# Performance work log

Measured on AMD Instinct MI355X. Metric: run time of the kernel, lower is better.

## Reference

```python
import jax, jax.numpy as jnp
import numpy as np

NUM_EMB = 512
LATENT = 20


def setup_inputs() -> dict:
    key = jax.random.key(0)
    ks = jax.random.split(key, 10)
    B = 262144
    c = jax.random.normal(ks[0], (B, 100), dtype=jnp.float32)
    W1 = jax.random.normal(ks[1], (100, 200), dtype=jnp.float32) * 0.1
    b1 = jnp.zeros((200,), dtype=jnp.float32)
    W2 = jax.random.normal(ks[2], (200, LATENT), dtype=jnp.float32) * 0.07
    b2 = jnp.zeros((LATENT,), dtype=jnp.float32)
    # codebook initialized uniform(-1/K, 1/K) as in torch
    codebook = jax.random.uniform(ks[3], (NUM_EMB, LATENT), dtype=jnp.float32,
                                  minval=-1.0 / NUM_EMB, maxval=1.0 / NUM_EMB)
    Wmu = jax.random.normal(ks[4], (LATENT, LATENT), dtype=jnp.float32) * 0.2
    bmu = jnp.zeros((LATENT,), dtype=jnp.float32)
    Wlv = jax.random.normal(ks[5], (LATENT, LATENT), dtype=jnp.float32) * 0.2
    blv = jnp.zeros((LATENT,), dtype=jnp.float32)
    return {"c": c, "W1": W1, "b1": b1, "W2": W2, "b2": b2,
            "codebook": codebook, "Wmu": Wmu, "bmu": bmu, "Wlv": Wlv, "blv": blv}


def reference(c, W1, b1, W2, b2, codebook, Wmu, bmu, Wlv, blv):
    # encoder: Linear -> ELU -> Linear
    h = jax.nn.elu(c @ W1 + b1)            # [B, 200]
    z_e = h @ W2 + b2                      # [B, 20]

    # vector quantization: pairwise squared distances to codebook
    d = (jnp.sum(z_e ** 2, axis=1, keepdims=True)
         + jnp.sum(codebook ** 2, axis=1)
         - 2.0 * z_e @ codebook.T)         # [B, K]
    idx = jnp.argmin(d, axis=1)            # [B]
    quantized = codebook[idx]              # [B, 20] gather

    commitment_loss = 0.25 * jnp.mean((jax.lax.stop_gradient(quantized) - z_e) ** 2)
    quantization_loss = jnp.mean((quantized - jax.lax.stop_gradient(z_e)) ** 2)
    z_q = z_e + jax.lax.stop_gradient(quantized - z_e)  # straight-through

    mu_c = z_e @ Wmu + bmu
    logvar_c = z_e @ Wlv + blv
    return (mu_c, logvar_c, z_q, z_e, quantization_loss, commitment_loss)
```

## Files before the change

kernel.cpp:

```cpp
#include <hip/hip_runtime.h>

typedef __bf16 bf16x8 __attribute__((ext_vector_type(8)));
typedef __bf16 bf16x4 __attribute__((ext_vector_type(4)));
typedef float  f32x4  __attribute__((ext_vector_type(4)));
typedef float  f32x2  __attribute__((ext_vector_type(2)));

constexpr int BN  = 262144;
constexpr int DIN = 100;
constexpr int DH  = 200;
constexpr int DZ  = 20;
constexpr int KCB = 512;

constexpr size_t WS_W1F  = 0;
constexpr size_t WS_W2F  = 53248;
constexpr size_t WS_CBF  = 69632;
constexpr size_t WS_WMUF = 102400;
constexpr size_t WS_WLVF = 104448;
constexpr size_t WS_B1P  = 106496;
constexpr size_t WS_B2P  = 107520;
constexpr size_t WS_BMUP = 107648;
constexpr size_t WS_BLVP = 107776;
constexpr size_t WS_PART = 107904;

constexpr int PN_W1 = 26624, PN_W2 = 8192, PN_CB = 16384, PN_WMU = 1024, PN_WLV = 1024;
constexpr int PN_TOT = PN_W1 + PN_W2 + PN_CB + PN_WMU + PN_WLV + 256 + 32 + 32 + 32;

__device__ __forceinline__ unsigned umin2(unsigned a, unsigned b) { return a < b ? a : b; }

__global__ __launch_bounds__(256) void prep_kernel(
    const float* __restrict__ W1, const float* __restrict__ b1,
    const float* __restrict__ W2, const float* __restrict__ b2,
    const float* __restrict__ cb,
    const float* __restrict__ Wmu, const float* __restrict__ bmu,
    const float* __restrict__ Wlv, const float* __restrict__ blv,
    unsigned char* __restrict__ ws)
{
    int e = blockIdx.x * 256 + threadIdx.x;
    if (e >= PN_TOT) return;
    __bf16* w1f  = (__bf16*)(ws + WS_W1F);
    __bf16* w2f  = (__bf16*)(ws + WS_W2F);
    __bf16* cbf  = (__bf16*)(ws + WS_CBF);
    __bf16* wmuf = (__bf16*)(ws + WS_WMUF);
    __bf16* wlvf = (__bf16*)(ws + WS_WLVF);
    float* b1p  = (float*)(ws + WS_B1P);
    float* b2p  = (float*)(ws + WS_B2P);
    float* bmup = (float*)(ws + WS_BMUP);
    float* blvp = (float*)(ws + WS_BLVP);

    if (e < PN_W1) {
        int j = e & 7, lane = (e >> 3) & 63, kk = (e >> 9) & 3, m = e >> 11;
        int n = m * 16 + (lane & 15);
        int k = kk * 32 + ((lane >> 4) << 3) + j;
        w1f[e] = (__bf16)((n < DH && k < DIN) ? W1[k * DH + n] : 0.f);
        return;
    }
    e -= PN_W1;
    if (e < PN_W2) {
        int j = e & 7, lane = (e >> 3) & 63, kk = (e >> 9) & 7, m2 = e >> 12;
        int n = m2 * 16 + (lane & 15);
        int k = kk * 32 + ((lane >> 4) << 3) + j;
        w2f[e] = (__bf16)((n < DZ && k < DH) ? W2[k * DZ + n] : 0.f);
        return;
    }
    e -= PN_W2;
    if (e < PN_CB) {
        int j = e & 7, lane = (e >> 3) & 63, ct = e >> 9;
        int code = ct * 16 + (lane & 15);
        int d = ((lane >> 4) << 3) + j;
        float v = 0.f;
        if (d < DZ) v = -2.f * cb[code * DZ + d];
        else if (d == DZ) {
            float s = 0.f;
            #pragma unroll
            for (int dd = 0; dd < DZ; ++dd) s = fmaf(cb[code * DZ + dd], cb[code * DZ + dd], s);
            v = s;
        }
        cbf[e] = (__bf16)v;
        return;
    }
    e -= PN_CB;
    if (e < PN_WMU) {
        int j = e & 7, lane = (e >> 3) & 63, m2 = e >> 9;
        int n = m2 * 16 + (lane & 15);
        int k = ((lane >> 4) << 3) + j;
        wmuf[e] = (__bf16)((n < DZ && k < DZ) ? Wmu[k * DZ + n] : 0.f);
        return;
    }
    e -= PN_WMU;
    if (e < PN_WLV) {
        int j = e & 7, lane = (e >> 3) & 63, m2 = e >> 9;
        int n = m2 * 16 + (lane & 15);
        int k = ((lane >> 4) << 3) + j;
        wlvf[e] = (__bf16)((n < DZ && k < DZ) ? Wlv[k * DZ + n] : 0.f);
        return;
    }
    e -= PN_WLV;
    if (e < 256) { b1p[e] = (e < DH) ? b1[e] : 0.f; return; }
    e -= 256;
    if (e < 32) { b2p[e] = (e < DZ) ? b2[e] : 0.f; return; }
    e -= 32;
    if (e < 32) { bmup[e] = (e < DZ) ? bmu[e] : 0.f; return; }
    e -= 32;
    blvp[e - 32] = (e - 32 < DZ) ? blv[e - 32] : 0.f;
}

__global__ __launch_bounds__(128) void fused_main(
    const float* __restrict__ c, const float* __restrict__ cb,
    const unsigned char* __restrict__ ws, float* __restrict__ out,
    float* __restrict__ partials)
{
    __shared__ __align__(16) unsigned char region[16384];

    const __bf16* w1f  = (const __bf16*)(ws + WS_W1F);
    const __bf16* w2f  = (const __bf16*)(ws + WS_W2F);
    const __bf16* cbf  = (const __bf16*)(ws + WS_CBF);
    const __bf16* wmuf = (const __bf16*)(ws + WS_WMUF);
    const __bf16* wlvf = (const __bf16*)(ws + WS_WLVF);
    const float* b1p  = (const float*)(ws + WS_B1P);
    const float* b2p  = (const float*)(ws + WS_B2P);
    const float* bmup = (const float*)(ws + WS_BMUP);
    const float* blvp = (const float*)(ws + WS_BLVP);

    const int tid = threadIdx.x;
    const int l   = tid & 63;
    const int wid = __builtin_amdgcn_readfirstlane(tid >> 6);
    const int g   = l >> 4;
    const int li  = l & 15;
    const int rowB = blockIdx.x * 64;

    {
        const float4* cbase = (const float4*)(c + (size_t)rowB * DIN);
        #pragma unroll
        for (int i = 0; i < 13; ++i) {
            int f4 = tid + i * 128;
            if (i < 12 || tid < 64) {
                float4 v = cbase[f4];
                int row = f4 / 25;
                int k4  = (f4 - row * 25) * 4;
                bf16x4 p;
                p[0] = (__bf16)v.x; p[1] = (__bf16)v.y;
                p[2] = (__bf16)v.z; p[3] = (__bf16)v.w;
                int byte = (k4 * 2) ^ ((row & 7) << 4);
                *(bf16x4*)(region + row * 256 + byte) = p;
            }
        }
        #pragma unroll
        for (int i = 0; i < 4; ++i) {
            int e = tid + i * 128;
            if (e < 448) {
                int row = e / 7, s = e - row * 7;
                int byte = (200 + s * 8) ^ ((row & 7) << 4);
                *(uint2*)(region + row * 256 + byte) = uint2{0u, 0u};
            }
        }
    }
    __syncthreads();

    bf16x8 cf0[4], cf1[4];
    #pragma unroll
    for (int nt = 0; nt < 2; ++nt) {
        const int row = wid * 32 + nt * 16 + li;
        const unsigned char* rb = region + row * 256;
        const int swz = (row & 7) << 4;
        #pragma unroll
        for (int kk = 0; kk < 4; ++kk) {
            bf16x8 a = *(const bf16x8*)(rb + ((kk * 64 + g * 16) ^ swz));
            if (nt == 0) cf0[kk] = a; else cf1[kk] = a;
        }
    }

    f32x4 zm0n0, zm0n1, zm1n0, zm1n1;
    {
        f32x4 bz0 = *(const f32x4*)(b2p + g * 4);
        f32x4 bz1 = *(const f32x4*)(b2p + 16 + g * 4);
        zm0n0 = bz0; zm0n1 = bz0; zm1n0 = bz1; zm1n1 = bz1;
    }

    unsigned char* hW = region + wid * 8192;
    const int swzH = (li & 7) << 4;

    #pragma unroll
    for (int hf = 0; hf < 2; ++hf) {
        #pragma unroll
        for (int t = 0; t < 8; ++t) {
            const int mg = hf * 8 + t;
            const int cbyte = (t * 32 + g * 8) ^ swzH;
            if (mg <= 12) {
                f32x4 acc0 = *(const f32x4*)(b1p + mg * 16 + g * 4);
                f32x4 acc1 = acc0;
                #pragma unroll
                for (int kk = 0; kk < 4; ++kk) {
                    bf16x8 aw = *(const bf16x8*)(w1f + ((mg * 4 + kk) * 512 + l * 8));
                    acc0 = __builtin_amdgcn_mfma_f32_16x16x32_bf16(aw, cf0[kk], acc0, 0, 0, 0);
                    acc1 = __builtin_amdgcn_mfma_f32_16x16x32_bf16(aw, cf1[kk], acc1, 0, 0, 0);
                }
                bf16x4 p0, p1;
                #pragma unroll
                for (int r = 0; r < 4; ++r) {
                    float h0 = acc0[r]; h0 = h0 > 0.f ? h0 : (__expf(h0) - 1.f);
                    float h1 = acc1[r]; h1 = h1 > 0.f ? h1 : (__expf(h1) - 1.f);
                    p0[r] = (__bf16)h0; p1[r] = (__bf16)h1;
                }
                *(bf16x4*)(hW + li * 256 + cbyte)        = p0;
                *(bf16x4*)(hW + (li + 16) * 256 + cbyte) = p1;
            } else {
                *(uint2*)(hW + li * 256 + cbyte)        = uint2{0u, 0u};
                *(uint2*)(hW + (li + 16) * 256 + cbyte) = uint2{0u, 0u};
            }
        }
        #pragma unroll
        for (int kk = 0; kk < 4; ++kk) {
            const int kk2 = hf * 4 + kk;
            const int rb = (kk * 64 + g * 16) ^ swzH;
            bf16x8 hb0 = *(const bf16x8*)(hW + li * 256 + rb);
            bf16x8 hb1 = *(const bf16x8*)(hW + (li + 16) * 256 + rb);
            bf16x8 w20 = *(const bf16x8*)(w2f + ((0 * 8 + kk2) * 512 + l * 8));
            bf16x8 w21 = *(const bf16x8*)(w2f + ((1 * 8 + kk2) * 512 + l * 8));
            zm0n0 = __builtin_amdgcn_mfma_f32_16x16x32_bf16(w20, hb0, zm0n0, 0, 0, 0);
            zm0n1 = __builtin_amdgcn_mfma_f32_16x16x32_bf16(w20, hb1, zm0n1, 0, 0, 0);
            zm1n0 = __builtin_amdgcn_mfma_f32_16x16x32_bf16(w21, hb0, zm1n0, 0, 0, 0);
            zm1n1 = __builtin_amdgcn_mfma_f32_16x16x32_bf16(w21, hb1, zm1n1, 0, 0, 0);
        }
    }

    unsigned char* zB = hW;
    const int swzZ = (li & 3) << 4;
    {
        bf16x4 q;
        #pragma unroll
        for (int r = 0; r < 4; ++r) q[r] = (__bf16)zm0n0[r];
        *(bf16x4*)(zB + li * 64 + ((g * 8) ^ swzZ)) = q;
        #pragma unroll
        for (int r = 0; r < 4; ++r) q[r] = (__bf16)zm0n1[r];
        *(bf16x4*)(zB + (li + 16) * 64 + ((g * 8) ^ swzZ)) = q;
        bf16x4 t0;
        #pragma unroll
        for (int r = 0; r < 4; ++r) t0[r] = (__bf16)0.f;
        bf16x4 t1 = t0;
        if (g == 0) {
            #pragma unroll
            for (int r = 0; r < 4; ++r) { t0[r] = (__bf16)zm1n0[r]; t1[r] = (__bf16)zm1n1[r]; }
        } else if (g == 1) { t0[0] = (__bf16)1.0f; t1[0] = (__bf16)1.0f; }
        *(bf16x4*)(zB + li * 64 + ((32 + g * 8) ^ swzZ)) = t0;
        *(bf16x4*)(zB + (li + 16) * 64 + ((32 + g * 8) ^ swzZ)) = t1;
    }

    bf16x8 za0 = *(const bf16x8*)(zB + li * 64 + ((g * 16) ^ swzZ));
    bf16x8 za1 = *(const bf16x8*)(zB + (li + 16) * 64 + ((g * 16) ^ swzZ));
    __syncthreads();

    unsigned run0 = 0xFFFFFFFFu, run1 = 0xFFFFFFFFu;
    f32x4 one4;
    one4[0] = 1.f; one4[1] = 1.f; one4[2] = 1.f; one4[3] = 1.f;
    #pragma unroll 8
    for (int ct = 0; ct < 32; ++ct) {
        bf16x8 cf = *(const bf16x8*)(cbf + (ct * 512 + l * 8));
        f32x4 s0 = __builtin_amdgcn_mfma_f32_16x16x32_bf16(cf, za0, one4, 0, 0, 0);
        f32x4 s1 = __builtin_amdgcn_mfma_f32_16x16x32_bf16(cf, za1, one4, 0, 0, 0);
        const unsigned ib = (unsigned)(ct * 16 + g * 4);
        unsigned k0 = (__float_as_uint(s0[0]) & ~511u) | (ib + 0);
        unsigned k1 = (__float_as_uint(s0[1]) & ~511u) | (ib + 1);
        unsigned k2 = (__float_as_uint(s0[2]) & ~511u) | (ib + 2);
        unsigned k3 = (__float_as_uint(s0[3]) & ~511u) | (ib + 3);
        run0 = umin2(umin2(k0, k1), umin2(umin2(k2, k3), run0));
        k0 = (__float_as_uint(s1[0]) & ~511u) | (ib + 0);
        k1 = (__float_as_uint(s1[1]) & ~511u) | (ib + 1);
        k2 = (__float_as_uint(s1[2]) & ~511u) | (ib + 2);
        k3 = (__float_as_uint(s1[3]) & ~511u) | (ib + 3);
        run1 = umin2(umin2(k0, k1), umin2(umin2(k2, k3), run1));
    }
    run0 = umin2(run0, (unsigned)__shfl_xor((int)run0, 16, 64));
    run0 = umin2(run0, (unsigned)__shfl_xor((int)run0, 32, 64));
    run1 = umin2(run1, (unsigned)__shfl_xor((int)run1, 16, 64));
    run1 = umin2(run1, (unsigned)__shfl_xor((int)run1, 32, 64));
    const int idx0 = (int)(run0 & 511u);
    const int idx1 = (int)(run1 & 511u);

    const size_t SEC = (size_t)BN * DZ;
    const size_t obase = (size_t)rowB * DZ;
    float* o_mu = out + obase;
    float* o_lv = out + SEC + obase;
    float* o_zq = out + 2 * SEC + obase;
    float* o_ze = out + 3 * SEC + obase;

    float* sA = (float*)region;
    float* sB = (float*)region + 1280;
    const int r0 = wid * 32 + li, r1 = r0 + 16;

    {
        f32x4 bm0 = *(const f32x4*)(bmup + g * 4);
        f32x4 bm1 = *(const f32x4*)(bmup + 16 + g * 4);
        bf16x8 wm0 = *(const bf16x8*)(wmuf + (0 * 512 + l * 8));
        bf16x8 wm1 = *(const bf16x8*)(wmuf + (1 * 512 + l * 8));
        f32x4 a00 = __builtin_amdgcn_mfma_f32_16x16x32_bf16(wm0, za0, bm0, 0, 0, 0);
        f32x4 a01 = __builtin_amdgcn_mfma_f32_16x16x32_bf16(wm0, za1, bm0, 0, 0, 0);
        f32x4 a10 = __builtin_amdgcn_mfma_f32_16x16x32_bf16(wm1, za0, bm1, 0, 0, 0);
        f32x4 a11 = __builtin_amdgcn_mfma_f32_16x16x32_bf16(wm1, za1, bm1, 0, 0, 0);
        *(float4*)(sA + r0 * DZ + g * 4) = *(float4*)&a00;
        *(float4*)(sA + r1 * DZ + g * 4) = *(float4*)&a01;
        if (g == 0) {
            *(float4*)(sA + r0 * DZ + 16) = *(float4*)&a10;
            *(float4*)(sA + r1 * DZ + 16) = *(float4*)&a11;
        }
    }
    {
        f32x4 bv0 = *(const f32x4*)(blvp + g * 4);
        f32x4 bv1 = *(const f32x4*)(blvp + 16 + g * 4);
        bf16x8 wl0 = *(const bf16x8*)(wlvf + (0 * 512 + l * 8));
        bf16x8 wl1 = *(const bf16x8*)(wlvf + (1 * 512 + l * 8));
        f32x4 a00 = __builtin_amdgcn_mfma_f32_16x16x32_bf16(wl0, za0, bv0, 0, 0, 0);
        f32x4 a01 = __builtin_amdgcn_mfma_f32_16x16x32_bf16(wl0, za1, bv0, 0, 0, 0);
        f32x4 a10 = __builtin_amdgcn_mfma_f32_16x16x32_bf16(wl1, za0, bv1, 0, 0, 0);
        f32x4 a11 = __builtin_amdgcn_mfma_f32_16x16x32_bf16(wl1, za1, bv1, 0, 0, 0);
        *(float4*)(sB + r0 * DZ + g * 4) = *(float4*)&a00;
        *(float4*)(sB + r1 * DZ + g * 4) = *(float4*)&a01;
        if (g == 0) {
            *(float4*)(sB + r0 * DZ + 16) = *(float4*)&a10;
            *(float4*)(sB + r1 * DZ + 16) = *(float4*)&a11;
        }
    }
    __syncthreads();
    #pragma unroll
    for (int i = 0; i < 5; ++i) {
        int w = tid * 2 + i * 256;
        __builtin_nontemporal_store(*(const f32x2*)(sA + w), (f32x2*)(o_mu + w));
        __builtin_nontemporal_store(*(const f32x2*)(sB + w), (f32x2*)(o_lv + w));
    }
    __syncthreads();

    float lsum = 0.f;
    {
        float4 q00 = *(const float4*)(cb + idx0 * DZ + g * 4);
        float4 q10 = *(const float4*)(cb + idx1 * DZ + g * 4);
        *(float4*)(sA + r0 * DZ + g * 4) = q00;
        *(float4*)(sA + r1 * DZ + g * 4) = q10;
        *(float4*)(sB + r0 * DZ + g * 4) = *(float4*)&zm0n0;
        *(float4*)(sB + r1 * DZ + g * 4) = *(float4*)&zm0n1;
        float d;
        d = q00.x - zm0n0[0]; lsum = fmaf(d, d, lsum);
        d = q00.y - zm0n0[1]; lsum = fmaf(d, d, lsum);
        d = q00.z - zm0n0[2]; lsum = fmaf(d, d, lsum);
        d = q00.w - zm0n0[3]; lsum = fmaf(d, d, lsum);
        d = q10.x - zm0n1[0]; lsum = fmaf(d, d, lsum);
        d = q10.y - zm0n1[1]; lsum = fmaf(d, d, lsum);
        d = q10.z - zm0n1[2]; lsum = fmaf(d, d, lsum);
        d = q10.w - zm0n1[3]; lsum = fmaf(d, d, lsum);
        if (g == 0) {
            float4 qe0 = *(const float4*)(cb + idx0 * DZ + 16);
            float4 qe1 = *(const float4*)(cb + idx1 * DZ + 16);
            *(float4*)(sA + r0 * DZ + 16) = qe0;
            *(float4*)(sA + r1 * DZ + 16) = qe1;
            *(float4*)(sB + r0 * DZ + 16) = *(float4*)&zm1n0;
            *(float4*)(sB + r1 * DZ + 16) = *(float4*)&zm1n1;
            d = qe0.x - zm1n0[0]; lsum = fmaf(d, d, lsum);
            d = qe0.y - zm1n0[1]; lsum = fmaf(d, d, lsum);
            d = qe0.z - zm1n0[2]; lsum = fmaf(d, d, lsum);
            d = qe0.w - zm1n0[3]; lsum = fmaf(d, d, lsum);
            d = qe1.x - zm1n1[0]; lsum = fmaf(d, d, lsum);
            d = qe1.y - zm1n1[1]; lsum = fmaf(d, d, lsum);
            d = qe1.z - zm1n1[2]; lsum = fmaf(d, d, lsum);
            d = qe1.w - zm1n1[3]; lsum = fmaf(d, d, lsum);
        }
    }
    #pragma unroll
    for (int off = 32; off > 0; off >>= 1) lsum += __shfl_down(lsum, off, 64);
    if (l == 0) partials[blockIdx.x * 2 + wid] = lsum;
    __syncthreads();
    #pragma unroll
    for (int i = 0; i < 5; ++i) {
        int w = tid * 2 + i * 256;
        __builtin_nontemporal_store(*(const f32x2*)(sA + w), (f32x2*)(o_zq + w));
        __builtin_nontemporal_store(*(const f32x2*)(sB + w), (f32x2*)(o_ze + w));
    }
}

__global__ __launch_bounds__(256) void loss_reduce(const float* __restrict__ partials,
                                                   float* __restrict__ out_scalars) {
    int t = threadIdx.x;
    float s = 0.f;
    #pragma unroll
    for (int i = 0; i < 32; ++i) s += partials[t + 256 * i];
    #pragma unroll
    for (int off = 32; off > 0; off >>= 1) s += __shfl_down(s, off, 64);
    __shared__ float wsum[4];
    if ((t & 63) == 0) wsum[t >> 6] = s;
    __syncthreads();
    if (t == 0) {
        float total = (wsum[0] + wsum[1]) + (wsum[2] + wsum[3]);
        float ql = total / (float)((size_t)BN * DZ);
        out_scalars[0] = ql;
        out_scalars[1] = 0.25f * ql;
    }
}

extern "C" void kernel_launch(void* const* d_in, const int* in_sizes, int n_in,
                              void* d_out, int out_size, void* d_ws, size_t ws_size,
                              hipStream_t stream) {
    const float* c   = (const float*)d_in[0];
    const float* W1  = (const float*)d_in[1];
    const float* b1  = (const float*)d_in[2];
    const float* W2  = (const float*)d_in[3];
    const float* b2  = (const float*)d_in[4];
    const float* cb  = (const float*)d_in[5];
    const float* Wmu = (const float*)d_in[6];
    const float* bmu = (const float*)d_in[7];
    const float* Wlv = (const float*)d_in[8];
    const float* blv = (const float*)d_in[9];
    float* out = (float*)d_out;
    unsigned char* ws = (unsigned char*)d_ws;
    float* partials = (float*)(ws + WS_PART);

    prep_kernel<<<(PN_TOT + 255) / 256, 256, 0, stream>>>(
        W1, b1, W2, b2, cb, Wmu, bmu, Wlv, blv, ws);
    fused_main<<<BN / 64, 128, 0, stream>>>(c, cb, ws, out, partials);
    loss_reduce<<<1, 256, 0, stream>>>(partials, out + 4 * (size_t)BN * DZ);
}
```

Measured before the change: 84.99 us.

## Process 64 rows per wave to reuse weight and codebook fragments across four tiles

Doubles the rows per block from 64 to 128, so each wave handles four 16-row tiles instead of two. Each W1, W2 and codebook fragment loaded from global memory now feeds four MFMAs instead of two, halving per-row weight and codebook load traffic. The cost is more registers (16 input fragments, 8 accumulators), doubled LDS per block (32KB) and half as many blocks, which may lower occupancy and latency hiding. The loss reduction is resized to match the smaller partials array.

```diff
diff --git a/kernel.cpp b/kernel.cpp
--- a/kernel.cpp
+++ b/kernel.cpp
@@ -109,7 +109,7 @@
     const unsigned char* __restrict__ ws, float* __restrict__ out,
     float* __restrict__ partials)
 {
-    __shared__ __align__(16) unsigned char region[16384];
+    __shared__ __align__(16) unsigned char region[32768];
 
     const __bf16* w1f  = (const __bf16*)(ws + WS_W1F);
     const __bf16* w2f  = (const __bf16*)(ws + WS_W2F);
@@ -126,57 +126,52 @@
     const int wid = __builtin_amdgcn_readfirstlane(tid >> 6);
     const int g   = l >> 4;
     const int li  = l & 15;
-    const int rowB = blockIdx.x * 64;
+    const int rowB = blockIdx.x * 128;
 
     {
         const float4* cbase = (const float4*)(c + (size_t)rowB * DIN);
         #pragma unroll
-        for (int i = 0; i < 13; ++i) {
+        for (int i = 0; i < 25; ++i) {
             int f4 = tid + i * 128;
-            if (i < 12 || tid < 64) {
-                float4 v = cbase[f4];
-                int row = f4 / 25;
-                int k4  = (f4 - row * 25) * 4;
-                bf16x4 p;
-                p[0] = (__bf16)v.x; p[1] = (__bf16)v.y;
-                p[2] = (__bf16)v.z; p[3] = (__bf16)v.w;
-                int byte = (k4 * 2) ^ ((row & 7) << 4);
-                *(bf16x4*)(region + row * 256 + byte) = p;
-            }
-        }
-        #pragma unroll
-        for (int i = 0; i < 4; ++i) {
+            float4 v = cbase[f4];
+            int row = f4 / 25;
+            int k4  = (f4 - row * 25) * 4;
+            bf16x4 p;
+            p[0] = (__bf16)v.x; p[1] = (__bf16)v.y;
+            p[2] = (__bf16)v.z; p[3] = (__bf16)v.w;
+            int byte = (k4 * 2) ^ ((row & 7) << 4);
+            *(bf16x4*)(region + row * 256 + byte) = p;
+        }
+        #pragma unroll
+        for (int i = 0; i < 7; ++i) {
             int e = tid + i * 128;
-            if (e < 448) {
-                int row = e / 7, s = e - row * 7;
-                int byte = (200 + s * 8) ^ ((row & 7) << 4);
-                *(uint2*)(region + row * 256 + byte) = uint2{0u, 0u};
-            }
-        }
-    }
-    __syncthreads();
-
-    bf16x8 cf0[4], cf1[4];
-    #pragma unroll
-    for (int nt = 0; nt < 2; ++nt) {
-        const int row = wid * 32 + nt * 16 + li;
+            int row = e / 7, s = e - row * 7;
+            int byte = (200 + s * 8) ^ ((row & 7) << 4);
+            *(uint2*)(region + row * 256 + byte) = uint2{0u, 0u};
+        }
+    }
+    __syncthreads();
+
+    bf16x8 cf[4][4];
+    #pragma unroll
+    for (int nt = 0; nt < 4; ++nt) {
+        const int row = wid * 64 + nt * 16 + li;
         const unsigned char* rb = region + row * 256;
         const int swz = (row & 7) << 4;
         #pragma unroll
-        for (int kk = 0; kk < 4; ++kk) {
-            bf16x8 a = *(const bf16x8*)(rb + ((kk * 64 + g * 16) ^ swz));
-            if (nt == 0) cf0[kk] = a; else cf1[kk] = a;
-        }
-    }
-
-    f32x4 zm0n0, zm0n1, zm1n0, zm1n1;
+        for (int kk = 0; kk < 4; ++kk)
+            cf[nt][kk] = *(const bf16x8*)(rb + ((kk * 64 + g * 16) ^ swz));
+    }
+
+    f32x4 zm0[4], zm1[4];
     {
         f32x4 bz0 = *(const f32x4*)(b2p + g * 4);
         f32x4 bz1 = *(const f32x4*)(b2p + 16 + g * 4);
-        zm0n0 = bz0; zm0n1 = bz0; zm1n0 = bz1; zm1n1 = bz1;
-    }
-
-    unsigned char* hW = region + wid * 8192;
+        #pragma unroll
+        for (int nt = 0; nt < 4; ++nt) { zm0[nt] = bz0; zm1[nt] = bz1; }
+    }
+
+    unsigned char* hW = region + wid * 16384;
     const int swzH = (li & 7) << 4;
 
     #pragma unroll
@@ -186,95 +181,101 @@
             const int mg = hf * 8 + t;
             const int cbyte = (t * 32 + g * 8) ^ swzH;
             if (mg <= 12) {
-                f32x4 acc0 = *(const f32x4*)(b1p + mg * 16 + g * 4);
-                f32x4 acc1 = acc0;
+                f32x4 acc[4];
+                f32x4 bias = *(const f32x4*)(b1p + mg * 16 + g * 4);
+                #pragma unroll
+                for (int nt = 0; nt < 4; ++nt) acc[nt] = bias;
                 #pragma unroll
                 for (int kk = 0; kk < 4; ++kk) {
                     bf16x8 aw = *(const bf16x8*)(w1f + ((mg * 4 + kk) * 512 + l * 8));
-                    acc0 = __builtin_amdgcn_mfma_f32_16x16x32_bf16(aw, cf0[kk], acc0, 0, 0, 0);
-                    acc1 = __builtin_amdgcn_mfma_f32_16x16x32_bf16(aw, cf1[kk], acc1, 0, 0, 0);
+                    #pragma unroll
+                    for (int nt = 0; nt < 4; ++nt)
+                        acc[nt] = __builtin_amdgcn_mfma_f32_16x16x32_bf16(aw, cf[nt][kk], acc[nt], 0, 0, 0);
                 }
-                bf16x4 p0, p1;
                 #pragma unroll
-                for (int r = 0; r < 4; ++r) {
-                    float h0 = acc0[r]; h0 = h0 > 0.f ? h0 : (__expf(h0) - 1.f);
-                    float h1 = acc1[r]; h1 = h1 > 0.f ? h1 : (__expf(h1) - 1.f);
-                    p0[r] = (__bf16)h0; p1[r] = (__bf16)h1;
+                for (int nt = 0; nt < 4; ++nt) {
+                    bf16x4 p;
+                    #pragma unroll
+                    for (int r = 0; r < 4; ++r) {
+                        float h = acc[nt][r];
+                        h = h > 0.f ? h : (__expf(h) - 1.f);
+                        p[r] = (__bf16)h;
+                    }
+                    *(bf16x4*)(hW + (li + 16 * nt) * 256 + cbyte) = p;
                 }
-                *(bf16x4*)(hW + li * 256 + cbyte)        = p0;
-                *(bf16x4*)(hW + (li + 16) * 256 + cbyte) = p1;
             } else {
-                *(uint2*)(hW + li * 256 + cbyte)        = uint2{0u, 0u};
-                *(uint2*)(hW + (li + 16) * 256 + cbyte) = uint2{0u, 0u};
+                #pragma unroll
+                for (int nt = 0; nt < 4; ++nt)
+                    *(uint2*)(hW + (li + 16 * nt) * 256 + cbyte) = uint2{0u, 0u};
             }
         }
         #pragma unroll
         for (int kk = 0; kk < 4; ++kk) {
             const int kk2 = hf * 4 + kk;
             const int rb = (kk * 64 + g * 16) ^ swzH;
-            bf16x8 hb0 = *(const bf16x8*)(hW + li * 256 + rb);
-            bf16x8 hb1 = *(const bf16x8*)(hW + (li + 16) * 256 + rb);
             bf16x8 w20 = *(const bf16x8*)(w2f + ((0 * 8 + kk2) * 512 + l * 8));
             bf16x8 w21 = *(const bf16x8*)(w2f + ((1 * 8 + kk2) * 512 + l * 8));
-            zm0n0 = __builtin_amdgcn_mfma_f32_16x16x32_bf16(w20, hb0, zm0n0, 0, 0, 0);
-            zm0n1 = __builtin_amdgcn_mfma_f32_16x16x32_bf16(w20, hb1, zm0n1, 0, 0, 0);
-            zm1n0 = __builtin_amdgcn_mfma_f32_16x16x32_bf16(w21, hb0, zm1n0, 0, 0, 0);
-            zm1n1 = __builtin_amdgcn_mfma_f32_16x16x32_bf16(w21, hb1, zm1n1, 0, 0, 0);
+            #pragma unroll
+            for (int nt = 0; nt < 4; ++nt) {
+                bf16x8 hb = *(const bf16x8*)(hW + (li + 16 * nt) * 256 + rb);
+                zm0[nt] = __builtin_amdgcn_mfma_f32_16x16x32_bf16(w20, hb, zm0[nt], 0, 0, 0);
+                zm1[nt] = __builtin_amdgcn_mfma_f32_16x16x32_bf16(w21, hb, zm1[nt], 0, 0, 0);
+            }
         }
     }
 
     unsigned char* zB = hW;
     const int swzZ = (li & 3) << 4;
-    {
+    #pragma unroll
+    for (int nt = 0; nt < 4; ++nt) {
+        const int zr = (li + 16 * nt) * 64;
         bf16x4 q;
         #pragma unroll
-        for (int r = 0; r < 4; ++r) q[r] = (__bf16)zm0n0[r];
-        *(bf16x4*)(zB + li * 64 + ((g * 8) ^ swzZ)) = q;
-        #pragma unroll
-        for (int r = 0; r < 4; ++r) q[r] = (__bf16)zm0n1[r];
-        *(bf16x4*)(zB + (li + 16) * 64 + ((g * 8) ^ swzZ)) = q;
+        for (int r = 0; r < 4; ++r) q[r] = (__bf16)zm0[nt][r];
+        *(bf16x4*)(zB + zr + ((g * 8) ^ swzZ)) = q;
         bf16x4 t0;
         #pragma unroll
         for (int r = 0; r < 4; ++r) t0[r] = (__bf16)0.f;
-        bf16x4 t1 = t0;
         if (g == 0) {
             #pragma unroll
-            for (int r = 0; r < 4; ++r) { t0[r] = (__bf16)zm1n0[r]; t1[r] = (__bf16)zm1n1[r]; }
-        } else if (g == 1) { t0[0] = (__bf16)1.0f; t1[0] = (__bf16)1.0f; }
-        *(bf16x4*)(zB + li * 64 + ((32 + g * 8) ^ swzZ)) = t0;
-        *(bf16x4*)(zB + (li + 16) * 64 + ((32 + g * 8) ^ swzZ)) = t1;
-    }
-
-    bf16x8 za0 = *(const bf16x8*)(zB + li * 64 + ((g * 16) ^ swzZ));
-    bf16x8 za1 = *(const bf16x8*)(zB + (li + 16) * 64 + ((g * 16) ^ swzZ));
-    __syncthreads();
-
-    unsigned run0 = 0xFFFFFFFFu, run1 = 0xFFFFFFFFu;
+            for (int r = 0; r < 4; ++r) t0[r] = (__bf16)zm1[nt][r];
+        } else if (g == 1) { t0[0] = (__bf16)1.0f; }
+        *(bf16x4*)(zB + zr + ((32 + g * 8) ^ swzZ)) = t0;
+    }
+
+    bf16x8 za[4];
+    #pragma unroll
+    for (int nt = 0; nt < 4; ++nt)
+        za[nt] = *(const bf16x8*)(zB + (li + 16 * nt) * 64 + ((g * 16) ^ swzZ));
+    __syncthreads();
+
+    unsigned run[4];
+    #pragma unroll
+    for (int nt = 0; nt < 4; ++nt) run[nt] = 0xFFFFFFFFu;
     f32x4 one4;
     one4[0] = 1.f; one4[1] = 1.f; one4[2] = 1.f; one4[3] = 1.f;
     #pragma unroll 8
     for (int ct = 0; ct < 32; ++ct) {
-        bf16x8 cf = *(const bf16x8*)(cbf + (ct * 512 + l * 8));
-        f32x4 s0 = __builtin_amdgcn_mfma_f32_16x16x32_bf16(cf, za0, one4, 0, 0, 0);
-        f32x4 s1 = __builtin_amdgcn_mfma_f32_16x16x32_bf16(cf, za1, one4, 0, 0, 0);
+        bf16x8 cf_ = *(const bf16x8*)(cbf + (ct * 512 + l * 8));
         const unsigned ib = (unsigned)(ct * 16 + g * 4);
-        unsigned k0 = (__float_as_uint(s0[0]) & ~511u) | (ib + 0);
-        unsigned k1 = (__float_as_uint(s0[1]) & ~511u) | (ib + 1);
-        unsigned k2 = (__float_as_uint(s0[2]) & ~511u) | (ib + 2);
-        unsigned k3 = (__float_as_uint(s0[3]) & ~511u) | (ib + 3);
-        run0 = umin2(umin2(k0, k1), umin2(umin2(k2, k3), run0));
-        k0 = (__float_as_uint(s1[0]) & ~511u) | (ib + 0);
-        k1 = (__float_as_uint(s1[1]) & ~511u) | (ib + 1);
-        k2 = (__float_as_uint(s1[2]) & ~511u) | (ib + 2);
-        k3 = (__float_as_uint(s1[3]) & ~511u) | (ib + 3);
-        run1 = umin2(umin2(k0, k1), umin2(umin2(k2, k3), run1));
-    }
-    run0 = umin2(run0, (unsigned)__shfl_xor((int)run0, 16, 64));
-    run0 = umin2(run0, (unsigned)__shfl_xor((int)run0, 32, 64));
-    run1 = umin2(run1, (unsigned)__shfl_xor((int)run1, 16, 64));
-    run1 = umin2(run1, (unsigned)__shfl_xor((int)run1, 32, 64));
-    const int idx0 = (int)(run0 & 511u);
-    const int idx1 = (int)(run1 & 511u);
+        #pragma unroll
+        for (int nt = 0; nt < 4; ++nt) {
+            f32x4 s = __builtin_amdgcn_mfma_f32_16x16x32_bf16(cf_, za[nt], one4, 0, 0, 0);
+            unsigned k0 = (__float_as_uint(s[0]) & ~511u) | (ib + 0);
+            unsigned k1 = (__float_as_uint(s[1]) & ~511u) | (ib + 1);
+            unsigned k2 = (__float_as_uint(s[2]) & ~511u) | (ib + 2);
+            unsigned k3 = (__float_as_uint(s[3]) & ~511u) | (ib + 3);
+            run[nt] = umin2(umin2(k0, k1), umin2(umin2(k2, k3), run[nt]));
+        }
+    }
+    int idx[4];
+    #pragma unroll
+    for (int nt = 0; nt < 4; ++nt) {
+        unsigned r = run[nt];
+        r = umin2(r, (unsigned)__shfl_xor((int)r, 16, 64));
+        r = umin2(r, (unsigned)__shfl_xor((int)r, 32, 64));
+        idx[nt] = (int)(r & 511u);
+    }
 
     const size_t SEC = (size_t)BN * DZ;
     const size_t obase = (size_t)rowB * DZ;
@@ -284,44 +285,41 @@
     float* o_ze = out + 3 * SEC + obase;
 
     float* sA = (float*)region;
-    float* sB = (float*)region + 1280;
-    const int r0 = wid * 32 + li, r1 = r0 + 16;
+    float* sB = (float*)region + 2560;
 
     {
         f32x4 bm0 = *(const f32x4*)(bmup + g * 4);
         f32x4 bm1 = *(const f32x4*)(bmup + 16 + g * 4);
         bf16x8 wm0 = *(const bf16x8*)(wmuf + (0 * 512 + l * 8));
         bf16x8 wm1 = *(const bf16x8*)(wmuf + (1 * 512 + l * 8));
-        f32x4 a00 = __builtin_amdgcn_mfma_f32_16x16x32_bf16(wm0, za0, bm0, 0, 0, 0);
-        f32x4 a01 = __builtin_amdgcn_mfma_f32_16x16x32_bf16(wm0, za1, bm0, 0, 0, 0);
-        f32x4 a10 = __builtin_amdgcn_mfma_f32_16x16x32_bf16(wm1, za0, bm1, 0, 0, 0);
-        f32x4 a11 = __builtin_amdgcn_mfma_f32_16x16x32_bf16(wm1, za1, bm1, 0, 0, 0);
-        *(float4*)(sA + r0 * DZ + g * 4) = *(float4*)&a00;
-        *(float4*)(sA + r1 * DZ + g * 4) = *(float4*)&a01;
-        if (g == 0) {
-            *(float4*)(sA + r0 * DZ + 16) = *(float4*)&a10;
-            *(float4*)(sA + r1 * DZ + 16) = *(float4*)&a11;
-        }
-    }
-    {
+        #pragma unroll
+        for (int nt = 0; nt < 4; ++nt) {
+            const int rr = wid * 64 + nt * 16 + li;
+            f32x4 a0 = __builtin_amdgcn_mfma_f32_16x16x32_bf16(wm0, za[nt], bm0, 0, 0, 0);
+            *(float4*)(sA + rr * DZ + g * 4) = *(float4*)&a0;
+            if (g == 0) {
+                f32x4 a1 = __builtin_amdgcn_mfma_f32_16x16x32_bf16(wm1, za[nt], bm1, 0, 0, 0);
+                *(float4*)(sA + rr * DZ + 16) = *(float4*)&a1;
+            }
+        }
         f32x4 bv0 = *(const f32x4*)(blvp + g * 4);
         f32x4 bv1 = *(const f32x4*)(blvp + 16 + g * 4);
         bf16x8 wl0 = *(const bf16x8*)(wlvf + (0 * 512 + l * 8));
         bf16x8 wl1 = *(const bf16x8*)(wlvf + (1 * 512 + l * 8));
-        f32x4 a00 = __builtin_amdgcn_mfma_f32_16x16x32_bf16(wl0, za0, bv0, 0, 0, 0);
-        f32x4 a01 = __builtin_amdgcn_mfma_f32_16x16x32_bf16(wl0, za1, bv0, 0, 0, 0);
-        f32x4 a10 = __builtin_amdgcn_mfma_f32_16x16x32_bf16(wl1, za0, bv1, 0, 0, 0);
-        f32x4 a11 = __builtin_amdgcn_mfma_f32_16x16x32_bf16(wl1, za1, bv1, 0, 0, 0);
-        *(float4*)(sB + r0 * DZ + g * 4) = *(float4*)&a00;
-        *(float4*)(sB + r1 * DZ + g * 4) = *(float4*)&a01;
-        if (g == 0) {
-            *(float4*)(sB + r0 * DZ + 16) = *(float4*)&a10;
-            *(float4*)(sB + r1 * DZ + 16) = *(float4*)&a11;
-        }
-    }
-    __syncthreads();
-    #pragma unroll
-    for (int i = 0; i < 5; ++i) {
+        #pragma unroll
+        for (int nt = 0; nt < 4; ++nt) {
+            const int rr = wid * 64 + nt * 16 + li;
+            f32x4 a0 = __builtin_amdgcn_mfma_f32_16x16x32_bf16(wl0, za[nt], bv0, 0, 0, 0);
+            *(float4*)(sB + rr * DZ + g * 4) = *(float4*)&a0;
+            if (g == 0) {
+                f32x4 a1 = __builtin_amdgcn_mfma_f32_16x16x32_bf16(wl1, za[nt], bv1, 0, 0, 0);
+                *(float4*)(sB + rr * DZ + 16) = *(float4*)&a1;
+            }
+        }
+    }
+    __syncthreads();
+    #pragma unroll
+    for (int i = 0; i < 10; ++i) {
         int w = tid * 2 + i * 256;
         __builtin_nontemporal_store(*(const f32x2*)(sA + w), (f32x2*)(o_mu + w));
         __builtin_nontemporal_store(*(const f32x2*)(sB + w), (f32x2*)(o_lv + w));
@@ -329,37 +327,25 @@
     __syncthreads();
 
     float lsum = 0.f;
-    {
-        float4 q00 = *(const float4*)(cb + idx0 * DZ + g * 4);
-        float4 q10 = *(const float4*)(cb + idx1 * DZ + g * 4);
-        *(float4*)(sA + r0 * DZ + g * 4) = q00;
-        *(float4*)(sA + r1 * DZ + g * 4) = q10;
-        *(float4*)(sB + r0 * DZ + g * 4) = *(float4*)&zm0n0;
-        *(float4*)(sB + r1 * DZ + g * 4) = *(float4*)&zm0n1;
+    #pragma unroll
+    for (int nt = 0; nt < 4; ++nt) {
+        const int rr = wid * 64 + nt * 16 + li;
+        float4 q0 = *(const float4*)(cb + idx[nt] * DZ + g * 4);
+        *(float4*)(sA + rr * DZ + g * 4) = q0;
+        *(float4*)(sB + rr * DZ + g * 4) = *(float4*)&zm0[nt];
         float d;
-        d = q00.x - zm0n0[0]; lsum = fmaf(d, d, lsum);
-        d = q00.y - zm0n0[1]; lsum = fmaf(d, d, lsum);
-        d = q00.z - zm0n0[2]; lsum = fmaf(d, d, lsum);
-        d = q00.w - zm0n0[3]; lsum = fmaf(d, d, lsum);
-        d = q10.x - zm0n1[0]; lsum = fmaf(d, d, lsum);
-        d = q10.y - zm0n1[1]; lsum = fmaf(d, d, lsum);
-        d = q10.z - zm0n1[2]; lsum = fmaf(d, d, lsum);
-        d = q10.w - zm0n1[3]; lsum = fmaf(d, d, lsum);
+        d = q0.x - zm0[nt][0]; lsum = fmaf(d, d, lsum);
+        d = q0.y - zm0[nt][1]; lsum = fmaf(d, d, lsum);
+        d = q0.z - zm0[nt][2]; lsum = fmaf(d, d, lsum);
+        d = q0.w - zm0[nt][3]; lsum = fmaf(d, d, lsum);
         if (g == 0) {
-            float4 qe0 = *(const float4*)(cb + idx0 * DZ + 16);
-            float4 qe1 = *(const float4*)(cb + idx1 * DZ + 16);
-            *(float4*)(sA + r0 * DZ + 16) = qe0;
-            *(float4*)(sA + r1 * DZ + 16) = qe1;
-            *(float4*)(sB + r0 * DZ + 16) = *(float4*)&zm1n0;
-            *(float4*)(sB + r1 * DZ + 16) = *(float4*)&zm1n1;
-            d = qe0.x - zm1n0[0]; lsum = fmaf(d, d, lsum);
-            d = qe0.y - zm1n0[1]; lsum = fmaf(d, d, lsum);
-            d = qe0.z - zm1n0[2]; lsum = fmaf(d, d, lsum);
-            d = qe0.w - zm1n0[3]; lsum = fmaf(d, d, lsum);
-            d = qe1.x - zm1n1[0]; lsum = fmaf(d, d, lsum);
-            d = qe1.y - zm1n1[1]; lsum = fmaf(d, d, lsum);
-            d = qe1.z - zm1n1[2]; lsum = fmaf(d, d, lsum);
-            d = qe1.w - zm1n1[3]; lsum = fmaf(d, d, lsum);
+            float4 qe = *(const float4*)(cb + idx[nt] * DZ + 16);
+            *(float4*)(sA + rr * DZ + 16) = qe;
+            *(float4*)(sB + rr * DZ + 16) = *(float4*)&zm1[nt];
+            d = qe.x - zm1[nt][0]; lsum = fmaf(d, d, lsum);
+            d = qe.y - zm1[nt][1]; lsum = fmaf(d, d, lsum);
+            d = qe.z - zm1[nt][2]; lsum = fmaf(d, d, lsum);
+            d = qe.w - zm1[nt][3]; lsum = fmaf(d, d, lsum);
         }
     }
     #pragma unroll
@@ -367,7 +353,7 @@
     if (l == 0) partials[blockIdx.x * 2 + wid] = lsum;
     __syncthreads();
     #pragma unroll
-    for (int i = 0; i < 5; ++i) {
+    for (int i = 0; i < 10; ++i) {
         int w = tid * 2 + i * 256;
         __builtin_nontemporal_store(*(const f32x2*)(sA + w), (f32x2*)(o_zq + w));
         __builtin_nontemporal_store(*(const f32x2*)(sB + w), (f32x2*)(o_ze + w));
@@ -379,7 +365,7 @@
     int t = threadIdx.x;
     float s = 0.f;
     #pragma unroll
-    for (int i = 0; i < 32; ++i) s += partials[t + 256 * i];
+    for (int i = 0; i < 16; ++i) s += partials[t + 256 * i];
     #pragma unroll
     for (int off = 32; off > 0; off >>= 1) s += __shfl_down(s, off, 64);
     __shared__ float wsum[4];
@@ -412,6 +398,6 @@
 
     prep_kernel<<<(PN_TOT + 255) / 256, 256, 0, stream>>>(
         W1, b1, W2, b2, cb, Wmu, bmu, Wlv, blv, ws);
-    fused_main<<<BN / 64, 128, 0, stream>>>(c, cb, ws, out, partials);
+    fused_main<<<BN / 128, 128, 0, stream>>>(c, cb, ws, out, partials);
     loss_reduce<<<1, 256, 0, stream>>>(partials, out + 4 * (size_t)BN * DZ);
 }
```

Measured after the change: 96.58 us. 1.14x slower.
